# Kernel optimization log

Hardware: AMD Instinct MI355X
Metric: run time of the kernel (lower is better)

## Reference

```python
import jax, jax.numpy as jnp
import numpy as np

B1, B2, D = 10000, 10000, 128
ORDER = 4


def _cdist(a, b):
    # Stable L2 distance matrix: (B1,B2)
    a2 = jnp.sum(a * a, axis=1)[:, None]
    b2 = jnp.sum(b * b, axis=1)[None, :]
    d2 = a2 + b2 - 2.0 * (a @ b.T)
    return jnp.sqrt(jnp.clip(d2, 0.0))


def setup_inputs() -> dict:
    key = jax.random.key(0)
    k1, k2, k3 = jax.random.split(key, 3)
    desc1 = jax.random.normal(k1, (B1, D), dtype=jnp.float32)
    desc2 = jax.random.normal(k2, (B2, D), dtype=jnp.float32)
    # Steerer generator (D,D); scaled so repeated application stays bounded.
    generator = jax.random.normal(k3, (D, D), dtype=jnp.float32) / np.sqrt(D)
    return {"desc1": desc1, "desc2": desc2, "generator": generator, "steerer_order": ORDER}


def reference(desc1, desc2, generator, steerer_order):
    # steer_mode='local': distance between a pair is the min over all
    # steered versions of desc1 (DiscreteSteerer applies F.linear(x, G),
    # i.e. x @ G.T, repeatedly).
    dm = _cdist(desc1, desc2)
    d = desc1
    for _ in range(steerer_order - 1):
        d = d @ generator.T
        dm = jnp.minimum(dm, _cdist(d, desc2))
    # match_mode='nn': nearest neighbor in desc2 for each row of desc1.
    match_dists = jnp.min(dm, axis=1)
    idxs_in_2 = jnp.argmin(dm, axis=1)
    idxs_in_1 = jnp.arange(dm.shape[0], dtype=jnp.int64 if jax.config.jax_enable_x64 else jnp.int32)
    matches_idxs = jnp.stack([idxs_in_1, idxs_in_2.astype(idxs_in_1.dtype)], axis=1)
    return match_dists[:, None], matches_idxs
```

## Files before the change

kernel.cpp:

```cpp
#include <hip/hip_runtime.h>
#include <hip/hip_fp16.h>
#include <math.h>

#define NB1 10000
#define NB2 10000
#define DD  128
#define NV  4
#define B1P 10016
#define B1R (B1P * NV)
#define NB2P 10112
#define NB2G 320
#define NJT 79
#define MB  128
#define BN  128
#define NCHUNK 4
#define SROWS 16
#define SCALE 64.0f

typedef _Float16 f16x8 __attribute__((ext_vector_type(8)));
typedef __attribute__((ext_vector_type(16))) float f32x16;

__device__ __forceinline__ void gload_lds16(const void* g, void* l) {
    __builtin_amdgcn_global_load_lds(
        (const __attribute__((address_space(1))) void*)g,
        (__attribute__((address_space(3))) void*)l, 16, 0, 0);
}
__device__ __forceinline__ f32x16 mfma16(f16x8 a, f16x8 b, f32x16 c) {
    return __builtin_amdgcn_mfma_f32_32x32x16_f16(a, b, c, 0, 0, 0);
}
__device__ __forceinline__ void enc(float x, unsigned short* hb, unsigned short* lb) {
    float xs = SCALE * x;
    __half hh = __float2half_rn(xs);
    __half hl = __float2half_rn(xs - __half2float(hh));
    *hb = __half_as_ushort(hh);
    *lb = __half_as_ushort(hl);
}
__device__ __forceinline__ size_t cmap(int row, int col) {
    return ((size_t)(row >> 5) * 16 + (col >> 4)) * 512
         + (size_t)((row & 31) + (((col >> 3) & 1) << 5)) * 8 + (col & 7);
}


__global__ void gt_kernel(const float* __restrict__ G, float* __restrict__ GT) {
    int idx = blockIdx.x * 256 + threadIdx.x;
    if (idx < DD * DD) {
        int c = idx / DD, f = idx % DD;
        GT[idx] = G[f * DD + c];
    }
}

__global__ void prep1_kernel(const float* __restrict__ desc1,
                             unsigned short* __restrict__ A2c, float* __restrict__ F0,
                             float* __restrict__ n1) {
    int i = blockIdx.x;
    int t = threadIdx.x;
    float x = (i < NB1) ? desc1[i * DD + t] : 0.f;
    F0[(size_t)i * DD + t] = x;
    unsigned short hb, lb;
    enc(x, &hb, &lb);
    int ar = i * NV;
    A2c[cmap(ar, t)] = hb;
    A2c[cmap(ar, 128 + t)] = lb;
    float s = x * x;
    for (int off = 32; off; off >>= 1) s += __shfl_down(s, off);
    __shared__ float p[2];
    if ((t & 63) == 0) p[t >> 6] = s;
    __syncthreads();
    if (t == 0) n1[i * NV] = p[0] + p[1];
}

__global__ void prep2_kernel(const float* __restrict__ desc2,
                             unsigned short* __restrict__ B2c, float* __restrict__ n2) {
    int j = blockIdx.x;
    int t = threadIdx.x;
    float x = (j < NB2) ? desc2[j * DD + t] : 0.f;
    unsigned short hb, lb;
    enc(x, &hb, &lb);
    B2c[cmap(j, t)] = hb;
    B2c[cmap(j, 128 + t)] = lb;
    float s = x * x;
    for (int off = 32; off; off >>= 1) s += __shfl_down(s, off);
    __shared__ float p[2];
    if ((t & 63) == 0) p[t >> 6] = s;
    __syncthreads();
    if (t == 0) n2[j] = (j < NB2) ? (p[0] + p[1]) : 1e30f;
}

__global__ void steer_kernel(float* __restrict__ F, unsigned short* __restrict__ A2c,
                             const float* __restrict__ GT, float* __restrict__ n1, int k) {
    __shared__ float src[SROWS][DD];
    int i0 = blockIdx.x * SROWS;
    int t = threadIdx.x;
    for (int r = 0; r < SROWS; ++r)
        src[r][t] = F[(size_t)(i0 + r) * DD + t];
    __syncthreads();
    float out[SROWS];
#pragma unroll
    for (int r = 0; r < SROWS; ++r) out[r] = 0.f;
    for (int c = 0; c < DD; ++c) {
        float g = GT[c * DD + t];
#pragma unroll
        for (int r = 0; r < SROWS; ++r) out[r] = fmaf(src[r][c], g, out[r]);
    }
    __shared__ float p2[SROWS][2];
    for (int r = 0; r < SROWS; ++r) {
        F[(size_t)(i0 + r) * DD + t] = out[r];
        unsigned short hb, lb;
        enc(out[r], &hb, &lb);
        int ar = (i0 + r) * NV + k;
        A2c[cmap(ar, t)] = hb;
        A2c[cmap(ar, 128 + t)] = lb;
        float s = out[r] * out[r];
        for (int off = 32; off; off >>= 1) s += __shfl_down(s, off);
        if ((t & 63) == 0) p2[r][t >> 6] = s;
    }
    __syncthreads();
    if (t < SROWS) n1[(i0 + t) * NV + k] = p2[t][0] + p2[t][1];
}


#define STAGEPH(BSEL, J0V, C16B, HALF)                                            \
    {                                                                             \
        _Pragma("unroll")                                                         \
        for (int c_ = 0; c_ < 2; ++c_) {                                          \
            int chunk_ = w * 2 + c_;                                              \
            int k16h_ = chunk_ >> 2, nf_ = chunk_ & 3;                            \
            size_t gc_ = (size_t)(((J0V) >> 5) + nf_) * 16 + (C16B) + (HALF) * 2 + k16h_; \
            gload_lds16((const char*)B2c + gc_ * 1024 + l * 16,                   \
                        LDSB + (BSEL) * 8192 + chunk_ * 1024 + l * 16);           \
        }                                                                         \
    }

#define COMP2(BSEL, HALF, AK0, AK1)                                               \
    {                                                                             \
        _Pragma("unroll")                                                         \
        for (int kh_ = 0; kh_ < 2; ++kh_) {                                       \
            f16x8 b0_ = *(const f16x8*)(LDSB + (BSEL) * 8192 + (kh_ * 4 + wn * 2 + 0) * 1024 + l * 16); \
            f16x8 b1_ = *(const f16x8*)(LDSB + (BSEL) * 8192 + (kh_ * 4 + wn * 2 + 1) * 1024 + l * 16); \
            acc[0][0] = mfma16(Areg[0][AK0][(HALF) * 2 + kh_], b0_, acc[0][0]);   \
            acc[0][1] = mfma16(Areg[0][AK0][(HALF) * 2 + kh_], b1_, acc[0][1]);   \
            acc[1][0] = mfma16(Areg[1][AK0][(HALF) * 2 + kh_], b0_, acc[1][0]);   \
            acc[1][1] = mfma16(Areg[1][AK0][(HALF) * 2 + kh_], b1_, acc[1][1]);   \
            acc[0][0] = mfma16(Areg[0][AK1][(HALF) * 2 + kh_], b0_, acc[0][0]);   \
            acc[0][1] = mfma16(Areg[0][AK1][(HALF) * 2 + kh_], b1_, acc[0][1]);   \
            acc[1][0] = mfma16(Areg[1][AK1][(HALF) * 2 + kh_], b0_, acc[1][0]);   \
            acc[1][1] = mfma16(Areg[1][AK1][(HALF) * 2 + kh_], b1_, acc[1][1]);   \
        }                                                                         \
    }

#define COMP1(BSEL, HALF, AK0)                                                    \
    {                                                                             \
        _Pragma("unroll")                                                         \
        for (int kh_ = 0; kh_ < 2; ++kh_) {                                       \
            f16x8 b0_ = *(const f16x8*)(LDSB + (BSEL) * 8192 + (kh_ * 4 + wn * 2 + 0) * 1024 + l * 16); \
            f16x8 b1_ = *(const f16x8*)(LDSB + (BSEL) * 8192 + (kh_ * 4 + wn * 2 + 1) * 1024 + l * 16); \
            acc[0][0] = mfma16(Areg[0][AK0][(HALF) * 2 + kh_], b0_, acc[0][0]);   \
            acc[0][1] = mfma16(Areg[0][AK0][(HALF) * 2 + kh_], b1_, acc[0][1]);   \
            acc[1][0] = mfma16(Areg[1][AK0][(HALF) * 2 + kh_], b0_, acc[1][0]);   \
            acc[1][1] = mfma16(Areg[1][AK0][(HALF) * 2 + kh_], b1_, acc[1][1]);   \
        }                                                                         \
    }

__global__ __launch_bounds__(256, 2) void match_kernel(
    const unsigned short* __restrict__ A2c, const unsigned short* __restrict__ B2c,
    const float* __restrict__ n1, const float* __restrict__ n2,
    float* __restrict__ pb, int* __restrict__ pj) {
    __shared__ __align__(16) char LDSB[16384];
    __shared__ float LDSn1[128];
    const int t = threadIdx.x;
    const int l = t & 63, w = t >> 6;
    const int wm = w >> 1, wn = w & 1;
    const int c5 = l & 31, h = l >> 5;
    const int bi = blockIdx.x, ch = blockIdx.y;
    const int R0 = bi * MB;

    f16x8 Areg[2][4][4];
#pragma unroll
    for (int a = 0; a < 2; ++a)
#pragma unroll
        for (int aks = 0; aks < 4; ++aks)
#pragma unroll
            for (int k16 = 0; k16 < 4; ++k16) {
                size_t g = (size_t)(bi * 4 + wm * 2 + a);
                Areg[a][aks][k16] = *(const f16x8*)(
                    (const char*)A2c + (g * 16 + aks * 4 + k16) * 1024 + l * 16);
            }

    const int jt0 = (ch * NJT) / NCHUNK;
    const int jt1 = ((ch + 1) * NJT) / NCHUNK;

    STAGEPH(0, jt0 * BN, 0, 0);
    if (t < 128) LDSn1[t] = n1[R0 + t];
    __syncthreads();

    float best[2][4];
    int bj[2][4];
#pragma unroll
    for (int a = 0; a < 2; ++a)
#pragma unroll
        for (int rq = 0; rq < 4; ++rq) { best[a][rq] = 3.4e38f; bj[a][rq] = 0; }

    for (int jt = jt0; jt < jt1; ++jt) {
        const int j0 = jt * BN;
        f32x16 acc[2][2];
#pragma unroll
        for (int a = 0; a < 2; ++a)
#pragma unroll
            for (int b = 0; b < 2; ++b)
#pragma unroll
                for (int e = 0; e < 16; ++e) acc[a][b][e] = 0.f;

        STAGEPH(1, j0, 0, 1);       COMP2(0, 0, 0, 2); __syncthreads();
        STAGEPH(0, j0, 4, 0);       COMP2(1, 1, 0, 2); __syncthreads();
        STAGEPH(1, j0, 4, 1);       COMP2(0, 0, 1, 3); __syncthreads();
        STAGEPH(0, j0, 8, 0);       COMP2(1, 1, 1, 3); __syncthreads();
        STAGEPH(1, j0, 8, 1);       COMP1(0, 0, 0);    __syncthreads();
        STAGEPH(0, j0, 12, 0);      COMP1(1, 1, 0);    __syncthreads();
        STAGEPH(1, j0, 12, 1);      COMP1(0, 0, 1);    __syncthreads();
        STAGEPH(0, j0 + BN, 0, 0);  COMP1(1, 1, 1);    __syncthreads();

        float nn0 = n2[j0 + wn * 64 + c5];
        float nn1 = n2[j0 + wn * 64 + 32 + c5];
#pragma unroll
        for (int a = 0; a < 2; ++a)
#pragma unroll
            for (int b = 0; b < 2; ++b) {
                float nn = b ? nn1 : nn0;
                int j = j0 + wn * 64 + b * 32 + c5;
#pragma unroll
                for (int rq = 0; rq < 4; ++rq) {
                    float4 n1v = *(const float4*)&LDSn1[(wm * 2 + a) * 32 + 8 * rq + 4 * h];
                    float e0 = fmaf(-0.00048828125f, acc[a][b][4 * rq + 0], n1v.x);
                    float e1 = fmaf(-0.00048828125f, acc[a][b][4 * rq + 1], n1v.y);
                    float e2 = fmaf(-0.00048828125f, acc[a][b][4 * rq + 2], n1v.z);
                    float e3 = fmaf(-0.00048828125f, acc[a][b][4 * rq + 3], n1v.w);
                    float d = fminf(fminf(e0, e1), fminf(e2, e3)) + nn;
                    if (d < best[a][rq]) { best[a][rq] = d; bj[a][rq] = j; }
                }
            }
    }

#pragma unroll
    for (int off = 1; off < 32; off <<= 1) {
#pragma unroll
        for (int a = 0; a < 2; ++a)
#pragma unroll
            for (int rq = 0; rq < 4; ++rq) {
                float ov = __shfl_xor(best[a][rq], off);
                int oj = __shfl_xor(bj[a][rq], off);
                if (ov < best[a][rq] || (ov == best[a][rq] && oj < bj[a][rq])) {
                    best[a][rq] = ov; bj[a][rq] = oj;
                }
            }
    }
    if (c5 == 0) {
        int slot = ch * 2 + wn;
#pragma unroll
        for (int a = 0; a < 2; ++a)
#pragma unroll
            for (int rq = 0; rq < 4; ++rq) {
                int i = bi * 32 + (wm * 2 + a) * 8 + 2 * rq + h;
                pb[slot * B1P + i] = best[a][rq];
                pj[slot * B1P + i] = bj[a][rq];
            }
    }
}

__global__ void final_kernel(const float* __restrict__ pb, const int* __restrict__ pj,
                             float* __restrict__ out) {
    int i = blockIdx.x * 256 + threadIdx.x;
    if (i < NB1) {
        float bv = 3.4e38f;
        int bj = 0;
#pragma unroll
        for (int s = 0; s < 2 * NCHUNK; ++s) {
            float v = pb[s * B1P + i];
            int j = pj[s * B1P + i];
            if (v < bv || (v == bv && j < bj)) { bv = v; bj = j; }
        }
        out[i] = sqrtf(fmaxf(bv, 0.f));
        out[NB1 + 2 * i] = (float)i;
        out[NB1 + 2 * i + 1] = (float)bj;
    }
}


extern "C" void kernel_launch(void* const* d_in, const int* in_sizes, int n_in,
                              void* d_out, int out_size, void* d_ws, size_t ws_size,
                              hipStream_t stream) {
    const float* desc1 = (const float*)d_in[0];
    const float* desc2 = (const float*)d_in[1];
    const float* G     = (const float*)d_in[2];

    unsigned short* A2c = (unsigned short*)d_ws;
    unsigned short* B2c = A2c + (size_t)(B1R / 32) * 16 * 512;
    float* F0 = (float*)(B2c + (size_t)NB2G * 16 * 512);
    float* GT = F0 + (size_t)B1P * DD;
    float* n1 = GT + DD * DD;
    float* n2 = n1 + B1R;
    float* pb = n2 + NB2P;
    int*   pj = (int*)(pb + 2 * NCHUNK * B1P);
    float* out = (float*)d_out;

    hipLaunchKernelGGL(gt_kernel, dim3((DD * DD + 255) / 256), dim3(256), 0, stream, G, GT);
    hipLaunchKernelGGL(prep1_kernel, dim3(B1P), dim3(DD), 0, stream, desc1, A2c, F0, n1);
    hipLaunchKernelGGL(prep2_kernel, dim3(NB2P), dim3(DD), 0, stream, desc2, B2c, n2);
    for (int k = 1; k < NV; ++k)
        hipLaunchKernelGGL(steer_kernel, dim3(B1P / SROWS), dim3(DD), 0, stream,
                           F0, A2c, GT, n1, k);
    hipLaunchKernelGGL(match_kernel, dim3(B1R / MB, NCHUNK), dim3(256), 0, stream,
                       A2c, B2c, n1, n2, pb, pj);
    hipLaunchKernelGGL(final_kernel, dim3((NB1 + 255) / 256), dim3(256), 0, stream,
                       pb, pj, out);
}
```

Baseline: 443.5 us.

## Fuse steering prep into one kernel and deepen match pipeline with 512-thread blocks

Merges the transpose, initial encode and three steer passes into a single kernel that holds G transposed in LDS and keeps the steered rows in shared memory, removing four launches and the F0/GT round trips through global memory. The match kernel moves to 512 threads per block covering 256 rows, with a 4-buffer LDS ring, explicit vmcnt waits plus s_barrier in place of __syncthreads, and more j-chunks. This is meant to cut launch and global-memory overhead and to overlap B-tile loads with MFMA work more deeply. In exchange it uses more LDS per block, which may lower occupancy, and the hand-tuned waitcnt scheme has to be exactly right to stay correct.

```diff
diff --git a/kernel.cpp b/kernel.cpp
--- a/kernel.cpp
+++ b/kernel.cpp
@@ -6,14 +6,14 @@
 #define NB2 10000
 #define DD  128
 #define NV  4
-#define B1P 10016
+#define B1P 10048
 #define B1R (B1P * NV)
 #define NB2P 10112
 #define NB2G 320
 #define NJT 79
-#define MB  128
+#define MB  256
 #define BN  128
-#define NCHUNK 4
+#define NCHUNK 6
 #define SROWS 16
 #define SCALE 64.0f
 
@@ -41,32 +41,49 @@
 }
 
 
-__global__ void gt_kernel(const float* __restrict__ G, float* __restrict__ GT) {
-    int idx = blockIdx.x * 256 + threadIdx.x;
-    if (idx < DD * DD) {
-        int c = idx / DD, f = idx % DD;
-        GT[idx] = G[f * DD + c];
-    }
-}
-
-__global__ void prep1_kernel(const float* __restrict__ desc1,
-                             unsigned short* __restrict__ A2c, float* __restrict__ F0,
-                             float* __restrict__ n1) {
-    int i = blockIdx.x;
-    int t = threadIdx.x;
-    float x = (i < NB1) ? desc1[i * DD + t] : 0.f;
-    F0[(size_t)i * DD + t] = x;
-    unsigned short hb, lb;
-    enc(x, &hb, &lb);
-    int ar = i * NV;
-    A2c[cmap(ar, t)] = hb;
-    A2c[cmap(ar, 128 + t)] = lb;
-    float s = x * x;
-    for (int off = 32; off; off >>= 1) s += __shfl_down(s, off);
-    __shared__ float p[2];
-    if ((t & 63) == 0) p[t >> 6] = s;
+__global__ __launch_bounds__(128) void prep1s_kernel(
+    const float* __restrict__ desc1, const float* __restrict__ G,
+    unsigned short* __restrict__ A2c, float* __restrict__ n1) {
+    __shared__ float GTl[128 * 129];
+    __shared__ float src[SROWS][DD];
+    __shared__ float p2[SROWS][2];
+    const int t = threadIdx.x;
+    const int i0 = blockIdx.x * SROWS;
+    for (int f = 0; f < DD; ++f)
+        GTl[t * 129 + f] = G[(size_t)f * DD + t];
+    for (int r = 0; r < SROWS; ++r)
+        src[r][t] = (i0 + r < NB1) ? desc1[(size_t)(i0 + r) * DD + t] : 0.f;
     __syncthreads();
-    if (t == 0) n1[i * NV] = p[0] + p[1];
+    for (int k = 0; k < NV; ++k) {
+        if (k > 0) {
+            float out[SROWS];
+#pragma unroll
+            for (int r = 0; r < SROWS; ++r) out[r] = 0.f;
+            for (int c = 0; c < DD; ++c) {
+                float g = GTl[c * 129 + t];
+#pragma unroll
+                for (int r = 0; r < SROWS; ++r) out[r] = fmaf(src[r][c], g, out[r]);
+            }
+            __syncthreads();
+#pragma unroll
+            for (int r = 0; r < SROWS; ++r) src[r][t] = out[r];
+            __syncthreads();
+        }
+        for (int r = 0; r < SROWS; ++r) {
+            float x = src[r][t];
+            unsigned short hb, lb;
+            enc(x, &hb, &lb);
+            int ar = (i0 + r) * NV + k;
+            A2c[cmap(ar, t)] = hb;
+            A2c[cmap(ar, 128 + t)] = lb;
+            float s = x * x;
+            for (int off = 32; off; off >>= 1) s += __shfl_down(s, off);
+            if ((t & 63) == 0) p2[r][t >> 6] = s;
+        }
+        __syncthreads();
+        if (t < SROWS) n1[(i0 + t) * NV + k] = p2[t][0] + p2[t][1];
+        __syncthreads();
+    }
 }
 
 __global__ void prep2_kernel(const float* __restrict__ desc2,
@@ -86,49 +103,13 @@
     if (t == 0) n2[j] = (j < NB2) ? (p[0] + p[1]) : 1e30f;
 }
 
-__global__ void steer_kernel(float* __restrict__ F, unsigned short* __restrict__ A2c,
-                             const float* __restrict__ GT, float* __restrict__ n1, int k) {
-    __shared__ float src[SROWS][DD];
-    int i0 = blockIdx.x * SROWS;
-    int t = threadIdx.x;
-    for (int r = 0; r < SROWS; ++r)
-        src[r][t] = F[(size_t)(i0 + r) * DD + t];
-    __syncthreads();
-    float out[SROWS];
-#pragma unroll
-    for (int r = 0; r < SROWS; ++r) out[r] = 0.f;
-    for (int c = 0; c < DD; ++c) {
-        float g = GT[c * DD + t];
-#pragma unroll
-        for (int r = 0; r < SROWS; ++r) out[r] = fmaf(src[r][c], g, out[r]);
-    }
-    __shared__ float p2[SROWS][2];
-    for (int r = 0; r < SROWS; ++r) {
-        F[(size_t)(i0 + r) * DD + t] = out[r];
-        unsigned short hb, lb;
-        enc(out[r], &hb, &lb);
-        int ar = (i0 + r) * NV + k;
-        A2c[cmap(ar, t)] = hb;
-        A2c[cmap(ar, 128 + t)] = lb;
-        float s = out[r] * out[r];
-        for (int off = 32; off; off >>= 1) s += __shfl_down(s, off);
-        if ((t & 63) == 0) p2[r][t >> 6] = s;
-    }
-    __syncthreads();
-    if (t < SROWS) n1[(i0 + t) * NV + k] = p2[t][0] + p2[t][1];
-}
-
-
-#define STAGEPH(BSEL, J0V, C16B, HALF)                                            \
+
+#define STAGE1(BSEL, J0V, C16B, HALF)                                             \
     {                                                                             \
-        _Pragma("unroll")                                                         \
-        for (int c_ = 0; c_ < 2; ++c_) {                                          \
-            int chunk_ = w * 2 + c_;                                              \
-            int k16h_ = chunk_ >> 2, nf_ = chunk_ & 3;                            \
-            size_t gc_ = (size_t)(((J0V) >> 5) + nf_) * 16 + (C16B) + (HALF) * 2 + k16h_; \
-            gload_lds16((const char*)B2c + gc_ * 1024 + l * 16,                   \
-                        LDSB + (BSEL) * 8192 + chunk_ * 1024 + l * 16);           \
-        }                                                                         \
+        int k16h_ = w >> 2, nf_ = w & 3;                                          \
+        size_t gc_ = (size_t)(((J0V) >> 5) + nf_) * 16 + (C16B) + (HALF) * 2 + k16h_; \
+        gload_lds16((const char*)B2c + gc_ * 1024 + l * 16,                       \
+                    LDSB + (BSEL) * 8192 + w * 1024 + l * 16);                    \
     }
 
 #define COMP2(BSEL, HALF, AK0, AK1)                                               \
@@ -161,12 +142,19 @@
         }                                                                         \
     }
 
-__global__ __launch_bounds__(256, 2) void match_kernel(
+#define PH(VM, BS, J0S, C16S, HS, CMP)                           \
+    asm volatile("s_waitcnt vmcnt(" VM ")" ::: "memory");        \
+    __builtin_amdgcn_s_barrier();                                \
+    __builtin_amdgcn_sched_barrier(0);                           \
+    STAGE1(BS, J0S, C16S, HS);                                   \
+    CMP
+
+__global__ __launch_bounds__(512, 2) void match_kernel(
     const unsigned short* __restrict__ A2c, const unsigned short* __restrict__ B2c,
     const float* __restrict__ n1, const float* __restrict__ n2,
     float* __restrict__ pb, int* __restrict__ pj) {
-    __shared__ __align__(16) char LDSB[16384];
-    __shared__ float LDSn1[128];
+    __shared__ __align__(16) char LDSB[4 * 8192];
+    __shared__ float LDSn1[256];
     const int t = threadIdx.x;
     const int l = t & 63, w = t >> 6;
     const int wm = w >> 1, wn = w & 1;
@@ -181,17 +169,19 @@
         for (int aks = 0; aks < 4; ++aks)
 #pragma unroll
             for (int k16 = 0; k16 < 4; ++k16) {
-                size_t g = (size_t)(bi * 4 + wm * 2 + a);
+                size_t g = (size_t)(bi * 8 + wm * 2 + a);
                 Areg[a][aks][k16] = *(const f16x8*)(
                     (const char*)A2c + (g * 16 + aks * 4 + k16) * 1024 + l * 16);
             }
+    { int idx = t & 255; LDSn1[idx] = n1[R0 + idx]; }
 
     const int jt0 = (ch * NJT) / NCHUNK;
     const int jt1 = ((ch + 1) * NJT) / NCHUNK;
 
-    STAGEPH(0, jt0 * BN, 0, 0);
-    if (t < 128) LDSn1[t] = n1[R0 + t];
-    __syncthreads();
+    STAGE1(0, jt0 * BN, 0, 0);
+    STAGE1(1, jt0 * BN, 0, 1);
+    STAGE1(2, jt0 * BN, 4, 0);
+    asm volatile("s_waitcnt lgkmcnt(0)" ::: "memory");
 
     float best[2][4];
     int bj[2][4];
@@ -202,25 +192,25 @@
 
     for (int jt = jt0; jt < jt1; ++jt) {
         const int j0 = jt * BN;
-        f32x16 acc[2][2];
-#pragma unroll
-        for (int a = 0; a < 2; ++a)
-#pragma unroll
-            for (int b = 0; b < 2; ++b)
-#pragma unroll
-                for (int e = 0; e < 16; ++e) acc[a][b][e] = 0.f;
-
-        STAGEPH(1, j0, 0, 1);       COMP2(0, 0, 0, 2); __syncthreads();
-        STAGEPH(0, j0, 4, 0);       COMP2(1, 1, 0, 2); __syncthreads();
-        STAGEPH(1, j0, 4, 1);       COMP2(0, 0, 1, 3); __syncthreads();
-        STAGEPH(0, j0, 8, 0);       COMP2(1, 1, 1, 3); __syncthreads();
-        STAGEPH(1, j0, 8, 1);       COMP1(0, 0, 0);    __syncthreads();
-        STAGEPH(0, j0, 12, 0);      COMP1(1, 1, 0);    __syncthreads();
-        STAGEPH(1, j0, 12, 1);      COMP1(0, 0, 1);    __syncthreads();
-        STAGEPH(0, j0 + BN, 0, 0);  COMP1(1, 1, 1);    __syncthreads();
-
         float nn0 = n2[j0 + wn * 64 + c5];
         float nn1 = n2[j0 + wn * 64 + 32 + c5];
+        f32x16 acc[2][2];
+#pragma unroll
+        for (int a = 0; a < 2; ++a)
+#pragma unroll
+            for (int b = 0; b < 2; ++b)
+#pragma unroll
+                for (int e = 0; e < 16; ++e) acc[a][b][e] = 0.f;
+
+        PH("4", 3, j0, 4, 1,       COMP2(0, 0, 0, 2));
+        PH("4", 0, j0, 8, 0,       COMP2(1, 1, 0, 2));
+        PH("4", 1, j0, 8, 1,       COMP2(2, 0, 1, 3));
+        PH("2", 2, j0, 12, 0,      COMP2(3, 1, 1, 3));
+        PH("2", 3, j0, 12, 1,      COMP1(0, 0, 0));
+        PH("2", 0, j0 + BN, 0, 0,  COMP1(1, 1, 0));
+        PH("2", 1, j0 + BN, 0, 1,  COMP1(2, 0, 1));
+        PH("2", 2, j0 + BN, 4, 0,  COMP1(3, 1, 1));
+
 #pragma unroll
         for (int a = 0; a < 2; ++a)
 #pragma unroll
@@ -229,7 +219,7 @@
                 int j = j0 + wn * 64 + b * 32 + c5;
 #pragma unroll
                 for (int rq = 0; rq < 4; ++rq) {
-                    float4 n1v = *(const float4*)&LDSn1[(wm * 2 + a) * 32 + 8 * rq + 4 * h];
+                    float4 n1v = *(const float4*)&LDSn1[wm * 64 + a * 32 + 8 * rq + 4 * h];
                     float e0 = fmaf(-0.00048828125f, acc[a][b][4 * rq + 0], n1v.x);
                     float e1 = fmaf(-0.00048828125f, acc[a][b][4 * rq + 1], n1v.y);
                     float e2 = fmaf(-0.00048828125f, acc[a][b][4 * rq + 2], n1v.z);
@@ -259,7 +249,7 @@
         for (int a = 0; a < 2; ++a)
 #pragma unroll
             for (int rq = 0; rq < 4; ++rq) {
-                int i = bi * 32 + (wm * 2 + a) * 8 + 2 * rq + h;
+                int i = bi * 64 + wm * 16 + a * 8 + 2 * rq + h;
                 pb[slot * B1P + i] = best[a][rq];
                 pj[slot * B1P + i] = bj[a][rq];
             }
@@ -294,21 +284,16 @@
 
     unsigned short* A2c = (unsigned short*)d_ws;
     unsigned short* B2c = A2c + (size_t)(B1R / 32) * 16 * 512;
-    float* F0 = (float*)(B2c + (size_t)NB2G * 16 * 512);
-    float* GT = F0 + (size_t)B1P * DD;
-    float* n1 = GT + DD * DD;
+    float* n1 = (float*)(B2c + (size_t)NB2G * 16 * 512);
     float* n2 = n1 + B1R;
     float* pb = n2 + NB2P;
     int*   pj = (int*)(pb + 2 * NCHUNK * B1P);
     float* out = (float*)d_out;
 
-    hipLaunchKernelGGL(gt_kernel, dim3((DD * DD + 255) / 256), dim3(256), 0, stream, G, GT);
-    hipLaunchKernelGGL(prep1_kernel, dim3(B1P), dim3(DD), 0, stream, desc1, A2c, F0, n1);
-    hipLaunchKernelGGL(prep2_kernel, dim3(NB2P), dim3(DD), 0, stream, desc2, B2c, n2);
-    for (int k = 1; k < NV; ++k)
-        hipLaunchKernelGGL(steer_kernel, dim3(B1P / SROWS), dim3(DD), 0, stream,
-                           F0, A2c, GT, n1, k);
-    hipLaunchKernelGGL(match_kernel, dim3(B1R / MB, NCHUNK), dim3(256), 0, stream,
+    hipLaunchKernelGGL(prep1s_kernel, dim3(B1P / SROWS), dim3(128), 0, stream,
+                       desc1, G, A2c, n1);
+    hipLaunchKernelGGL(prep2_kernel, dim3(NB2P), dim3(128), 0, stream, desc2, B2c, n2);
+    hipLaunchKernelGGL(match_kernel, dim3(B1R / MB, NCHUNK), dim3(512), 0, stream,
                        A2c, B2c, n1, n2, pb, pj);
     hipLaunchKernelGGL(final_kernel, dim3((NB1 + 255) / 256), dim3(256), 0, stream,
                        pb, pj, out);
```

Measured after the change: 455.2 us. +2.6%, slower.
